# Optimization experiments

Hardware: AMD Instinct MI355X
Metric: run time of the kernel (lower is better)

## Reference

```python
import jax, jax.numpy as jnp
import numpy as np

B, S, T = 4, 1024, 1024
HID, ATT, NH = 1024, 1024, 16
HD = ATT // NH  # head size 64


def setup_inputs() -> dict:
    key = jax.random.key(0)
    ks = jax.random.split(key, 12)
    sc = 1.0 / np.sqrt(HID)
    return {
        "src": jax.random.normal(ks[0], (B, S, HID), jnp.float32),
        "tgt": jax.random.normal(ks[1], (B, T, HID), jnp.float32),
        "src_mask": jax.random.randint(ks[2], (B, S), 0, 2) > 0,
        "tgt_mask": jax.random.randint(ks[3], (B, T), 0, 2) > 0,
        "qw": jax.random.normal(ks[4], (ATT, HID), jnp.float32) * sc,
        "qb": jnp.zeros((ATT,), jnp.float32),
        "kw": jax.random.normal(ks[5], (ATT, HID), jnp.float32) * sc,
        "kb": jnp.zeros((ATT,), jnp.float32),
        "vw": jax.random.normal(ks[6], (ATT, HID), jnp.float32) * sc,
        "vb": jnp.zeros((ATT,), jnp.float32),
        "ow": jax.random.normal(ks[7], (HID, ATT), jnp.float32) * (1.0 / np.sqrt(ATT)),
        "ob": jnp.zeros((HID,), jnp.float32),
    }


def _heads(x, w, b, L):
    # x:[B,L,HID] -> [B,NH,L,HD]
    return (x @ w.T + b).reshape(B, L, NH, HD).transpose(0, 2, 1, 3)


def reference(src, tgt, src_mask, tgt_mask, qw, qb, kw, kb, vw, vb, ow, ob):
    q = _heads(src, qw, qb, S)
    k = _heads(tgt, kw, kb, T)
    v_src = _heads(src, vw, vb, S)
    v_tgt = _heads(tgt, vw, vb, T)

    attn = jnp.einsum("bhsd,bhtd->bhst", q, k) / np.sqrt(HD)  # shared scores

    sm = src_mask[:, None, :, None].astype(attn.dtype)  # [B,1,S,1]
    tm = tgt_mask[:, None, None, :].astype(attn.dtype)  # [B,1,1,T]
    NEG = 100000.0
    attn_src = attn * sm - NEG * (1.0 - sm)
    attn_tgt = attn * tm - NEG * (1.0 - tm)

    p_src = jax.nn.softmax(attn_src, axis=-1)                        # [B,H,S,T]
    p_tgt = jax.nn.softmax(attn_tgt.swapaxes(-1, -2), axis=-1)       # [B,H,T,S]

    o_src = jnp.einsum("bhst,bhtd->bhsd", p_src, v_tgt)
    o_tgt = jnp.einsum("bhts,bhsd->bhtd", p_tgt, v_src)

    o_src = o_src.transpose(0, 2, 1, 3).reshape(B, S, ATT) @ ow.T + ob
    o_tgt = o_tgt.transpose(0, 2, 1, 3).reshape(B, T, ATT) @ ow.T + ob
    return (o_src, o_tgt)
```

## Files before the change

kernel.cpp:

```cpp
#include <hip/hip_runtime.h>
#include <stdint.h>

typedef _Float16 f16;
typedef _Float16 f16x8 __attribute__((ext_vector_type(8)));
typedef _Float16 f16x4 __attribute__((ext_vector_type(4)));
typedef float    f32x4 __attribute__((ext_vector_type(4)));

#define MFMA_F16(A, B, C) __builtin_amdgcn_mfma_f32_16x16x32_f16((A), (B), (C), 0, 0, 0)

__device__ __forceinline__ void gload_lds16(const void* g, void* l) {
  __builtin_amdgcn_global_load_lds((const __attribute__((address_space(1))) void*)g,
                                   (__attribute__((address_space(3))) void*)l, 16, 0, 0);
}

__global__ void cvt_f32_f16(const float* __restrict__ s0, const float* __restrict__ s1,
                            const float* __restrict__ s2, const float* __restrict__ s3,
                            const float* __restrict__ s4, const float* __restrict__ s5,
                            f16* __restrict__ d0, f16* __restrict__ d1, f16* __restrict__ d2,
                            f16* __restrict__ d3, f16* __restrict__ d4, f16* __restrict__ d5) {
  const float* sp; f16* dp; int n4;
  switch (blockIdx.y) {
    case 0:  sp = s0; dp = d0; n4 = (4096 * 1024) / 4; break;
    case 1:  sp = s1; dp = d1; n4 = (4096 * 1024) / 4; break;
    case 2:  sp = s2; dp = d2; n4 = (1024 * 1024) / 4; break;
    case 3:  sp = s3; dp = d3; n4 = (1024 * 1024) / 4; break;
    case 4:  sp = s4; dp = d4; n4 = (1024 * 1024) / 4; break;
    default: sp = s5; dp = d5; n4 = (1024 * 1024) / 4; break;
  }
  int stride = gridDim.x * blockDim.x;
  for (int i = blockIdx.x * blockDim.x + threadIdx.x; i < n4; i += stride) {
    f32x4 v = *(const f32x4*)(sp + (size_t)i * 4);
    f16x4 h;
    h[0] = (f16)v[0]; h[1] = (f16)v[1]; h[2] = (f16)v[2]; h[3] = (f16)v[3];
    *(f16x4*)(dp + (size_t)i * 4) = h;
  }
}

__device__ __forceinline__ void gemm_core_k1024(const f16* __restrict__ A, const f16* __restrict__ W,
                                                f16* lA, f16* lB, f32x4 (&acc)[4][4],
                                                int row0, int col0) {
  const int tid = threadIdx.x;
  const int lane = tid & 63;
  const int w = tid >> 6;
  const int g = lane >> 4, c = lane & 15;
  const int wr = (w >> 1) * 64, wc = (w & 1) * 64;

  int sr[2], scol[2];
#pragma unroll
  for (int p = 0; p < 2; ++p) {
    int slot = p * 256 + tid;
    int r = slot >> 2, sph = slot & 3;
    sr[p] = r;
    scol[p] = (sph ^ ((r >> 1) & 3)) * 8;
  }
  const f16* Abase = A + (size_t)row0 * 1024;
  const f16* Wbase = W + (size_t)col0 * 1024;

  auto STAGE = [&](int nb, int k0) {
#pragma unroll
    for (int p = 0; p < 2; ++p) {
      gload_lds16(Abase + (size_t)sr[p] * 1024 + k0 + scol[p],
                  lA + nb * (128 * 32) + (p * 256 + w * 64) * 8);
      gload_lds16(Wbase + (size_t)sr[p] * 1024 + k0 + scol[p],
                  lB + nb * (128 * 32) + (p * 256 + w * 64) * 8);
    }
  };

  STAGE(0, 0);

  for (int kt = 0; kt < 32; ++kt) {
    const int cur = kt & 1;
    asm volatile("s_waitcnt vmcnt(0)" ::: "memory");
    __builtin_amdgcn_s_barrier();
    __builtin_amdgcn_sched_barrier(0);
    if (kt < 31) STAGE(cur ^ 1, (kt + 1) * 32);

    const f16* cA = lA + cur * (128 * 32);
    const f16* cB = lB + cur * (128 * 32);
    f16x8 af[4], bf[4];
#pragma unroll
    for (int m = 0; m < 4; ++m) {
      int r = wr + m * 16 + c;
      af[m] = *(const f16x8*)(cA + r * 32 + (g ^ ((r >> 1) & 3)) * 8);
    }
#pragma unroll
    for (int n = 0; n < 4; ++n) {
      int r = wc + n * 16 + c;
      bf[n] = *(const f16x8*)(cB + r * 32 + (g ^ ((r >> 1) & 3)) * 8);
    }
    __builtin_amdgcn_s_setprio(1);
#pragma unroll
    for (int m = 0; m < 4; ++m)
#pragma unroll
      for (int n = 0; n < 4; ++n)
        acc[m][n] = MFMA_F16(af[m], bf[n], acc[m][n]);
    __builtin_amdgcn_s_setprio(0);
  }
}

__global__ __launch_bounds__(256, 2) void proj_gemm(
    const f16* __restrict__ src16, const f16* __restrict__ tgt16,
    const f16* __restrict__ qw16, const f16* __restrict__ kw16, const f16* __restrict__ vw16,
    const float* __restrict__ qb, const float* __restrict__ kb, const float* __restrict__ vb,
    f16* __restrict__ q16, f16* __restrict__ k16, f16* __restrict__ vtS, f16* __restrict__ vtT) {
  __shared__ f16 lA[2 * 128 * 32];
  __shared__ f16 lB[2 * 128 * 32];
  const int lin = blockIdx.x;
  const int xcd = lin & 7;
  const int slot = lin >> 3;
  const int z = xcd >> 1;
  const int y = (xcd & 1) * 16 + (slot >> 3);
  const int x = slot & 7;

  const f16* A = (z & 1) ? tgt16 : src16;
  const f16* W = (z == 0) ? qw16 : (z == 1) ? kw16 : vw16;
  const float* bias = (z == 0) ? qb : (z == 1) ? kb : vb;
  const int row0 = y * 128;
  const int col0 = x * 128;
  f32x4 acc[4][4] = {};
  gemm_core_k1024(A, W, lA, lB, acc, row0, col0);

  const int lane = threadIdx.x & 63;
  const int w = threadIdx.x >> 6;
  const int g = lane >> 4, c = lane & 15;
  const int wr = (w >> 1) * 64, wc = (w & 1) * 64;

  if (z < 2) {
    f16* O = (z == 0) ? q16 : k16;
#pragma unroll
    for (int n = 0; n < 4; ++n) {
      int colg = col0 + wc + n * 16 + c;
      float bv = bias[colg];
#pragma unroll
      for (int m = 0; m < 4; ++m) {
        int rb = row0 + wr + m * 16 + g * 4;
#pragma unroll
        for (int r = 0; r < 4; ++r)
          O[(size_t)(rb + r) * 1024 + colg] = (f16)(acc[m][n][r] + bv);
      }
    }
  } else {
    f16* O = (z == 2) ? vtS : vtT;
#pragma unroll
    for (int n = 0; n < 4; ++n) {
      int colg = col0 + wc + n * 16 + c;
      float bv = bias[colg];
#pragma unroll
      for (int m = 0; m < 4; ++m) {
        int row = row0 + wr + m * 16 + g * 4;
        int bb = row >> 10, t = row & 1023;
        int tl = t & 63;
        int tp = (t & ~63) + (tl & 32) + ((tl & 12) << 1) + ((tl & 16) >> 2) + (tl & 3);
        f16x4 pk;
#pragma unroll
        for (int r = 0; r < 4; ++r) pk[r] = (f16)(acc[m][n][r] + bv);
        *(f16x4*)(O + ((size_t)(bb << 10) + colg) * 1024 + tp) = pk;
      }
    }
  }
}

__global__ __launch_bounds__(256, 2) void out_gemm(
    const f16* __restrict__ opre, const f16* __restrict__ ow16,
    const float* __restrict__ ob, float* __restrict__ out) {
  __shared__ f16 lA[2 * 128 * 32];
  __shared__ f16 lB[2 * 128 * 32];
  const int lin = blockIdx.x;
  const int xcd = lin & 7;
  const int slot = lin >> 3;
  const int y = xcd * 8 + (slot >> 3);
  const int x = slot & 7;
  const int row0 = y * 128;
  const int col0 = x * 128;
  f32x4 acc[4][4] = {};
  gemm_core_k1024(opre, ow16, lA, lB, acc, row0, col0);
  const int lane = threadIdx.x & 63;
  const int w = threadIdx.x >> 6;
  const int g = lane >> 4, c = lane & 15;
  const int wr = (w >> 1) * 64, wc = (w & 1) * 64;
#pragma unroll
  for (int n = 0; n < 4; ++n) {
    int colg = col0 + wc + n * 16 + c;
    float bv = ob[colg];
#pragma unroll
    for (int m = 0; m < 4; ++m) {
      int rb = row0 + wr + m * 16 + g * 4;
#pragma unroll
      for (int r = 0; r < 4; ++r)
        out[(size_t)(rb + r) * 1024 + colg] = acc[m][n][r] + bv;
    }
  }
}

__global__ __launch_bounds__(256, 2) void attn_fwd(
    const f16* __restrict__ q16, const f16* __restrict__ k16,
    const f16* __restrict__ vtS, const f16* __restrict__ vtT,
    const int* __restrict__ smask, const int* __restrict__ tmask,
    f16* __restrict__ opre) {
  const int bid = blockIdx.x;
  const int xcd = bid & 7;
  const int idx = bid >> 3;
  const int bhp = xcd * 16 + (idx >> 2);
  const int qblk = idx & 3;
  const int pass = bhp >> 6;
  const int bh = bhp & 63;
  const int b = bh >> 4, h = bh & 15;

  const f16* Q  = pass ? k16 : q16;
  const f16* Kt = pass ? q16 : k16;
  const f16* VT = pass ? vtS : vtT;
  const int* qmask = pass ? tmask : smask;
  const int outRowOff = pass ? 4096 : 0;

  const int tid = threadIdx.x;
  const int lane = tid & 63, wv = tid >> 6;
  const int g = lane >> 4, c = lane & 15;
  const int qrow0 = qblk * 256 + wv * 64;

  __shared__ f16 lK[2][64 * 64];
  __shared__ f16 lV[2][64 * 64];

  const size_t kbase = (size_t)b * (1024 * 1024) + h * 64;
  const size_t vbase = (size_t)bh * (64 * 1024);

  const float SC2 = 0.18033688f;
  f16x8 qf[4][2];
#pragma unroll
  for (int m = 0; m < 4; ++m) {
    f16 sh = (f16)(qmask[b * 1024 + qrow0 + m * 16 + c] ? SC2 : 0.0f);
#pragma unroll
    for (int kc = 0; kc < 2; ++kc) {
      f16x8 v = *(const f16x8*)(Q + ((size_t)(b * 1024 + qrow0 + m * 16 + c)) * 1024 + h * 64 + kc * 32 + g * 8);
#pragma unroll
      for (int j = 0; j < 8; ++j) v[j] *= sh;
      qf[m][kc] = v;
    }
  }

  auto STAGE = [&](int nb, int t0) {
#pragma unroll
    for (int i = 0; i < 2; ++i) {
      int p = i * 256 + tid;
      int row = p >> 3;
      int u = (p & 7) ^ (row & 7);
      gload_lds16(Kt + kbase + (size_t)(t0 + row) * 1024 + u * 8, &lK[nb][(i * 256 + wv * 64) * 8]);
      gload_lds16(VT + vbase + (size_t)row * 1024 + t0 + u * 8, &lV[nb][(i * 256 + wv * 64) * 8]);
    }
  };

  f32x4 accO[4][4] = {};
  float lpart[4] = {0.0f, 0.0f, 0.0f, 0.0f};

  STAGE(0, 0);

  for (int tt = 0; tt < 16; ++tt) {
    asm volatile("s_waitcnt vmcnt(0)" ::: "memory");
    __builtin_amdgcn_s_barrier();
    __builtin_amdgcn_sched_barrier(0);
    if (tt < 15) STAGE((tt + 1) & 1, (tt + 1) * 64);
    const f16* curK = lK[tt & 1];
    const f16* curV = lV[tt & 1];

    f16x8 kf[4][2];
#pragma unroll
    for (int n = 0; n < 4; ++n) {
      int row = n * 16 + c;
#pragma unroll
      for (int kc = 0; kc < 2; ++kc)
        kf[n][kc] = *(const f16x8*)(curK + row * 64 + (((kc * 4 + g) ^ (row & 7)) * 8));
    }

    f16x8 pa[4][2];
#pragma unroll
    for (int m = 0; m < 4; ++m) {
      f32x4 sc[4];
      __builtin_amdgcn_s_setprio(1);
#pragma unroll
      for (int n = 0; n < 4; ++n) {
        f32x4 z = {0.0f, 0.0f, 0.0f, 0.0f};
        z = MFMA_F16(kf[n][0], qf[m][0], z);
        sc[n] = MFMA_F16(kf[n][1], qf[m][1], z);
      }
      __builtin_amdgcn_s_setprio(0);
      float e[16];
#pragma unroll
      for (int n = 0; n < 4; ++n)
#pragma unroll
        for (int r = 0; r < 4; ++r) e[n * 4 + r] = __builtin_amdgcn_exp2f(sc[n][r]);
      float s8[8];
#pragma unroll
      for (int i = 0; i < 8; ++i) s8[i] = e[i] + e[i + 8];
      float s4[4];
#pragma unroll
      for (int i = 0; i < 4; ++i) s4[i] = s8[i] + s8[i + 4];
      lpart[m] += (s4[0] + s4[1]) + (s4[2] + s4[3]);
#pragma unroll
      for (int kc = 0; kc < 2; ++kc) {
        f16x8 p8;
#pragma unroll
        for (int j = 0; j < 8; ++j) p8[j] = (f16)e[8 * kc + j];
        pa[m][kc] = p8;
      }
    }

    f16x8 vf[4][2];
#pragma unroll
    for (int nd = 0; nd < 4; ++nd) {
      int row = nd * 16 + c;
#pragma unroll
      for (int kc = 0; kc < 2; ++kc)
        vf[nd][kc] = *(const f16x8*)(curV + row * 64 + (((kc * 4 + g) ^ (row & 7)) * 8));
    }

    __builtin_amdgcn_s_setprio(1);
#pragma unroll
    for (int m = 0; m < 4; ++m)
#pragma unroll
      for (int nd = 0; nd < 4; ++nd) {
        accO[m][nd] = MFMA_F16(pa[m][0], vf[nd][0], accO[m][nd]);
        accO[m][nd] = MFMA_F16(pa[m][1], vf[nd][1], accO[m][nd]);
      }
    __builtin_amdgcn_s_setprio(0);
  }

#pragma unroll
  for (int m = 0; m < 4; ++m) {
    float ls = lpart[m];
    ls += __shfl_xor(ls, 16);
    ls += __shfl_xor(ls, 32);
#pragma unroll
    for (int r = 0; r < 4; ++r) {
      float lr = __shfl(ls, 20 * g + r);
      float inv = 1.0f / lr;
      size_t orow = (size_t)(outRowOff + b * 1024 + qrow0 + m * 16 + 4 * g + r);
#pragma unroll
      for (int nd = 0; nd < 4; ++nd)
        opre[orow * 1024 + h * 64 + nd * 16 + c] = (f16)(accO[m][nd][r] * inv);
    }
  }
}

extern "C" void kernel_launch(void* const* d_in, const int* in_sizes, int n_in,
                              void* d_out, int out_size, void* d_ws, size_t ws_size,
                              hipStream_t stream) {
  (void)in_sizes; (void)n_in; (void)out_size; (void)ws_size;
  const float* src = (const float*)d_in[0];
  const float* tgt = (const float*)d_in[1];
  const int*   smask = (const int*)d_in[2];
  const int*   tmask = (const int*)d_in[3];
  const float* qw = (const float*)d_in[4];
  const float* qb = (const float*)d_in[5];
  const float* kw = (const float*)d_in[6];
  const float* kb = (const float*)d_in[7];
  const float* vw = (const float*)d_in[8];
  const float* vb = (const float*)d_in[9];
  const float* ow = (const float*)d_in[10];
  const float* ob = (const float*)d_in[11];
  float* out = (float*)d_out;

  f16* wsp = (f16*)d_ws;
  const size_t M4 = (size_t)4096 * 1024;
  const size_t M1 = (size_t)1024 * 1024;
  f16* src16 = wsp;
  f16* tgt16 = src16 + M4;
  f16* qw16  = tgt16 + M4;
  f16* kw16  = qw16 + M1;
  f16* vw16  = kw16 + M1;
  f16* ow16  = vw16 + M1;
  f16* q16   = ow16 + M1;
  f16* k16   = q16 + M4;
  f16* vtS   = k16 + M4;
  f16* vtT   = vtS + M4;
  f16* opre  = wsp;

  cvt_f32_f16<<<dim3(512, 6), 256, 0, stream>>>(src, tgt, qw, kw, vw, ow,
                                                src16, tgt16, qw16, kw16, vw16, ow16);
  proj_gemm<<<dim3(1024), 256, 0, stream>>>(src16, tgt16, qw16, kw16, vw16,
                                            qb, kb, vb, q16, k16, vtS, vtT);
  attn_fwd<<<dim3(512), 256, 0, stream>>>(q16, k16, vtS, vtT, smask, tmask, opre);
  out_gemm<<<dim3(512), 256, 0, stream>>>(opre, ow16, ob, out);
}
```

Baseline: 127.0 us.

## Fuse Q/K and V projections per block to share the activation tile

The projection GEMM now has each block compute two output tiles, Q or K plus the matching V, from the same src/tgt A tile. It uses a second LDS buffer for the V weights and an inlined double-buffered K loop. This halves the grid and removes the duplicate loading of activation tiles that happened when Q/K and V were separate blocks. In exchange each block holds twice the accumulators and more LDS, which may lower occupancy below the launch-bounds target of 2 blocks per CU and may cause register spills.

```diff
diff --git a/kernel.cpp b/kernel.cpp
--- a/kernel.cpp
+++ b/kernel.cpp
@@ -104,58 +104,118 @@
     const float* __restrict__ qb, const float* __restrict__ kb, const float* __restrict__ vb,
     f16* __restrict__ q16, f16* __restrict__ k16, f16* __restrict__ vtS, f16* __restrict__ vtT) {
   __shared__ f16 lA[2 * 128 * 32];
-  __shared__ f16 lB[2 * 128 * 32];
+  __shared__ f16 lB1[2 * 128 * 32];
+  __shared__ f16 lB2[2 * 128 * 32];
   const int lin = blockIdx.x;
   const int xcd = lin & 7;
   const int slot = lin >> 3;
-  const int z = xcd >> 1;
-  const int y = (xcd & 1) * 16 + (slot >> 3);
+  const int pr = xcd >> 2;
+  const int y = (xcd & 3) * 8 + (slot >> 3);
   const int x = slot & 7;
 
-  const f16* A = (z & 1) ? tgt16 : src16;
-  const f16* W = (z == 0) ? qw16 : (z == 1) ? kw16 : vw16;
-  const float* bias = (z == 0) ? qb : (z == 1) ? kb : vb;
+  const f16* A  = pr ? tgt16 : src16;
+  const f16* W1 = pr ? kw16 : qw16;
+  const float* b1 = pr ? kb : qb;
+  f16* O1 = pr ? k16 : q16;
+  f16* O2 = pr ? vtT : vtS;
   const int row0 = y * 128;
   const int col0 = x * 128;
-  f32x4 acc[4][4] = {};
-  gemm_core_k1024(A, W, lA, lB, acc, row0, col0);
-
-  const int lane = threadIdx.x & 63;
-  const int w = threadIdx.x >> 6;
+
+  const int tid = threadIdx.x;
+  const int lane = tid & 63;
+  const int w = tid >> 6;
   const int g = lane >> 4, c = lane & 15;
   const int wr = (w >> 1) * 64, wc = (w & 1) * 64;
 
-  if (z < 2) {
-    f16* O = (z == 0) ? q16 : k16;
+  int sr[2], scol[2];
+#pragma unroll
+  for (int p = 0; p < 2; ++p) {
+    int slt = p * 256 + tid;
+    int r = slt >> 2, sph = slt & 3;
+    sr[p] = r;
+    scol[p] = (sph ^ ((r >> 1) & 3)) * 8;
+  }
+  const f16* Abase  = A + (size_t)row0 * 1024;
+  const f16* W1base = W1 + (size_t)col0 * 1024;
+  const f16* W2base = vw16 + (size_t)col0 * 1024;
+
+  auto STAGE = [&](int nb, int k0) {
+#pragma unroll
+    for (int p = 0; p < 2; ++p) {
+      gload_lds16(Abase + (size_t)sr[p] * 1024 + k0 + scol[p],
+                  lA + nb * (128 * 32) + (p * 256 + w * 64) * 8);
+      gload_lds16(W1base + (size_t)sr[p] * 1024 + k0 + scol[p],
+                  lB1 + nb * (128 * 32) + (p * 256 + w * 64) * 8);
+      gload_lds16(W2base + (size_t)sr[p] * 1024 + k0 + scol[p],
+                  lB2 + nb * (128 * 32) + (p * 256 + w * 64) * 8);
+    }
+  };
+
+  f32x4 acc1[4][4] = {};
+  f32x4 acc2[4][4] = {};
+
+  STAGE(0, 0);
+
+  for (int kt = 0; kt < 32; ++kt) {
+    const int cur = kt & 1;
+    asm volatile("s_waitcnt vmcnt(0)" ::: "memory");
+    __builtin_amdgcn_s_barrier();
+    __builtin_amdgcn_sched_barrier(0);
+    if (kt < 31) STAGE(cur ^ 1, (kt + 1) * 32);
+
+    const f16* cA = lA + cur * (128 * 32);
+    const f16* cB1 = lB1 + cur * (128 * 32);
+    const f16* cB2 = lB2 + cur * (128 * 32);
+    f16x8 af[4], bf1[4], bf2[4];
+#pragma unroll
+    for (int m = 0; m < 4; ++m) {
+      int r = wr + m * 16 + c;
+      af[m] = *(const f16x8*)(cA + r * 32 + (g ^ ((r >> 1) & 3)) * 8);
+    }
 #pragma unroll
     for (int n = 0; n < 4; ++n) {
-      int colg = col0 + wc + n * 16 + c;
-      float bv = bias[colg];
-#pragma unroll
-      for (int m = 0; m < 4; ++m) {
-        int rb = row0 + wr + m * 16 + g * 4;
-#pragma unroll
-        for (int r = 0; r < 4; ++r)
-          O[(size_t)(rb + r) * 1024 + colg] = (f16)(acc[m][n][r] + bv);
+      int r = wc + n * 16 + c;
+      int off = r * 32 + (g ^ ((r >> 1) & 3)) * 8;
+      bf1[n] = *(const f16x8*)(cB1 + off);
+      bf2[n] = *(const f16x8*)(cB2 + off);
+    }
+    __builtin_amdgcn_s_setprio(1);
+#pragma unroll
+    for (int m = 0; m < 4; ++m)
+#pragma unroll
+      for (int n = 0; n < 4; ++n) {
+        acc1[m][n] = MFMA_F16(af[m], bf1[n], acc1[m][n]);
+        acc2[m][n] = MFMA_F16(af[m], bf2[n], acc2[m][n]);
       }
-    }
-  } else {
-    f16* O = (z == 2) ? vtS : vtT;
-#pragma unroll
-    for (int n = 0; n < 4; ++n) {
-      int colg = col0 + wc + n * 16 + c;
-      float bv = bias[colg];
-#pragma unroll
-      for (int m = 0; m < 4; ++m) {
-        int row = row0 + wr + m * 16 + g * 4;
-        int bb = row >> 10, t = row & 1023;
-        int tl = t & 63;
-        int tp = (t & ~63) + (tl & 32) + ((tl & 12) << 1) + ((tl & 16) >> 2) + (tl & 3);
-        f16x4 pk;
-#pragma unroll
-        for (int r = 0; r < 4; ++r) pk[r] = (f16)(acc[m][n][r] + bv);
-        *(f16x4*)(O + ((size_t)(bb << 10) + colg) * 1024 + tp) = pk;
-      }
+    __builtin_amdgcn_s_setprio(0);
+  }
+
+#pragma unroll
+  for (int n = 0; n < 4; ++n) {
+    int colg = col0 + wc + n * 16 + c;
+    float bv = b1[colg];
+#pragma unroll
+    for (int m = 0; m < 4; ++m) {
+      int rb = row0 + wr + m * 16 + g * 4;
+#pragma unroll
+      for (int r = 0; r < 4; ++r)
+        O1[(size_t)(rb + r) * 1024 + colg] = (f16)(acc1[m][n][r] + bv);
+    }
+  }
+#pragma unroll
+  for (int n = 0; n < 4; ++n) {
+    int colg = col0 + wc + n * 16 + c;
+    float bv = vb[colg];
+#pragma unroll
+    for (int m = 0; m < 4; ++m) {
+      int row = row0 + wr + m * 16 + g * 4;
+      int bb = row >> 10, t = row & 1023;
+      int tl = t & 63;
+      int tp = (t & ~63) + (tl & 32) + ((tl & 12) << 1) + ((tl & 16) >> 2) + (tl & 3);
+      f16x4 pk;
+#pragma unroll
+      for (int r = 0; r < 4; ++r) pk[r] = (f16)(acc2[m][n][r] + bv);
+      *(f16x4*)(O2 + ((size_t)(bb << 10) + colg) * 1024 + tp) = pk;
     }
   }
 }
@@ -375,8 +435,8 @@
 
   cvt_f32_f16<<<dim3(512, 6), 256, 0, stream>>>(src, tgt, qw, kw, vw, ow,
                                                 src16, tgt16, qw16, kw16, vw16, ow16);
-  proj_gemm<<<dim3(1024), 256, 0, stream>>>(src16, tgt16, qw16, kw16, vw16,
-                                            qb, kb, vb, q16, k16, vtS, vtT);
+  proj_gemm<<<dim3(512), 256, 0, stream>>>(src16, tgt16, qw16, kw16, vw16,
+                                           qb, kb, vb, q16, k16, vtS, vtT);
   attn_fwd<<<dim3(512), 256, 0, stream>>>(q16, k16, vtS, vtT, smask, tmask, opre);
   out_gemm<<<dim3(512), 256, 0, stream>>>(opre, ow16, ob, out);
 }
```

Result: faster. 121.8 us (-4.0%).
